# Kernel tuning notes

Measured on AMD Instinct MI355X. Metric: run time of the kernel, lower is better.

The kernel has to match this reference:

```python
import jax, jax.numpy as jnp
import numpy as np

S, B, D_IN, D_SRC, D_ALIGN = 2048, 64, 512, 512, 512


def setup_inputs() -> dict:
    key = jax.random.key(0)
    ks = jax.random.split(key, 6)
    scale = 0.1  # matches uniform_(-0.1, 0.1) init magnitude
    return {
        "input": jax.random.normal(ks[0], (1, B, D_IN), dtype=jnp.float32),
        "source_hids": jax.random.normal(ks[1], (S, B, D_SRC), dtype=jnp.float32),
        "encoder_padding_mask": jnp.zeros((S, B), dtype=bool),
        "W1": jax.random.uniform(ks[2], (D_ALIGN, D_IN + D_SRC), jnp.float32, -scale, scale),
        "b1": jax.random.uniform(ks[3], (D_ALIGN,), jnp.float32, -scale, scale),
        "W2": jax.random.uniform(ks[4], (1, D_ALIGN), jnp.float32, -scale, scale),
        "b2": jax.random.uniform(ks[5], (1,), jnp.float32, -scale, scale),
    }


def reference(input, source_hids, encoder_padding_mask, W1, b1, W2, b2):
    # input: [1, B, D_in] broadcast over srclen; source_hids: [S, B, D_src]
    s = source_hids.shape[0]
    x = jnp.broadcast_to(input, (s,) + input.shape[1:])          # [S, B, D_in]
    cat = jnp.concatenate((x, source_hids), axis=-1)             # [S, B, D_in+D_src]
    h = jnp.tanh(jnp.einsum('sbd,ad->sba', cat, W1) + b1)        # [S, B, D_align]
    scores = jnp.einsum('sba,oa->sbo', h, W2)[..., 0] + b2[0]    # [S, B]
    scores = jnp.where(encoder_padding_mask, -jnp.inf, scores)
    attn = jax.nn.softmax(scores, axis=0)                        # softmax over srclen
    ctx = jnp.einsum('sb,sbd->bd', attn, source_hids)            # [B, D_src]
    return ctx, attn
```

## Files before the change

### kernel.cpp

```cpp
#include <hip/hip_runtime.h>
#include <hip/hip_bf16.h>
#include <math.h>

#define S_LEN 2048
#define BATCH 64
#define DDIM 512

typedef __attribute__((ext_vector_type(8))) short bf16x8;
typedef __attribute__((ext_vector_type(4))) float f32x4;
typedef __attribute__((ext_vector_type(4))) unsigned int u32x4;

typedef __attribute__((address_space(1))) const void g_void;
typedef __attribute__((address_space(3))) void l_void;

__device__ __forceinline__ unsigned short f2bf(float f) {
  unsigned int u = __float_as_uint(f);
  u += 0x7fffu + ((u >> 16) & 1u);
  return (unsigned short)(u >> 16);
}

__device__ __forceinline__ float tanh_fast(float x) {
  float e = __builtin_amdgcn_exp2f(x * 2.88539008177793f);
  return 1.0f - 2.0f * __builtin_amdgcn_rcpf(e + 1.0f);
}

__device__ __forceinline__ unsigned pkbf(float a, float b) {
  unsigned ua = __float_as_uint(a) + 0x8000u;
  unsigned ub = __float_as_uint(b) + 0x8000u;
  return __builtin_amdgcn_perm(ub, ua, 0x07060302u);
}

__global__ __launch_bounds__(256) void prep_kernel(
    const float* __restrict__ W1, const float* __restrict__ b1,
    const float* __restrict__ input, unsigned short* __restrict__ W1b,
    float* __restrict__ uprime) {
  __shared__ float w1row[1024];
  const int a = blockIdx.x;
  const int t = threadIdx.x;
  float4 v = *(const float4*)(W1 + a * 1024 + t * 4);
  *(float4*)(w1row + t * 4) = v;
  if (t >= 128) {
    ushort4 u;
    u.x = f2bf(v.x); u.y = f2bf(v.y); u.z = f2bf(v.z); u.w = f2bf(v.w);
    *(ushort4*)(W1b + a * 512 + (t * 4 - 512)) = u;
  }
  __syncthreads();
  if (t < BATCH) {
    const float4* inp = (const float4*)(input + t * 512);
    const float4* wr = (const float4*)w1row;
    float acc = b1[a];
#pragma unroll 4
    for (int d = 0; d < 128; ++d) {
      float4 x = inp[d], w = wr[d];
      acc += x.x * w.x + x.y * w.y + x.z * w.z + x.w * w.w;
    }
    uprime[t * 512 + a] = acc;
  }
}

__global__ __launch_bounds__(512, 2) void scores_kernel(
    const float* __restrict__ src, const unsigned short* __restrict__ W1b,
    const float* __restrict__ uprime, const float* __restrict__ W2,
    float* __restrict__ scores_t) {
  __shared__ unsigned short A_sm[128 * 64];
  __shared__ unsigned short B_sm[2 * 512 * 64];
  __shared__ float s_lds[128];

  const int t = threadIdx.x;
  const int sblk = blockIdx.x;
  const int w = t >> 6;
  const int lane = t & 63;
  const int quad = lane >> 4;
  const int l15 = lane & 15;

  if (t < 128) s_lds[t] = 0.f;

  f32x4 acc[8][4];
#pragma unroll
  for (int i = 0; i < 8; ++i)
#pragma unroll
    for (int j = 0; j < 4; ++j) acc[i][j] = (f32x4){0.f, 0.f, 0.f, 0.f};

  const int ar = t >> 2, aq = t & 3;
  const float* gA = src + (size_t)(sblk * 128) * DDIM + ar * DDIM + aq * 16;
  const int p0 = (2 * aq) ^ (ar & 7);
  const int p1 = (2 * aq + 1) ^ (ar & 7);
  unsigned short* ldsA0 = A_sm + ar * 64 + p0 * 8;
  unsigned short* ldsA1 = A_sm + ar * 64 + p1 * 8;

  const int br = lane >> 3, bp = lane & 7, bc = bp ^ (br & 7);
  const unsigned short* gBl = W1b + br * DDIM + bc * 8;

  {
    float4 as0 = ((const float4*)gA)[0];
    float4 as1 = ((const float4*)gA)[1];
    float4 as2 = ((const float4*)gA)[2];
    float4 as3 = ((const float4*)gA)[3];
#pragma unroll
    for (int g = 0; g < 8; ++g) {
      const unsigned short* gp = gBl + (g * 64 + w * 8) * DDIM;
      unsigned short* lp = B_sm + (g * 64 + w * 8) * 64;
      __builtin_amdgcn_global_load_lds((g_void*)gp, (l_void*)lp, 16, 0, 0);
    }
    u32x4 o0, o1;
    o0.x = pkbf(as0.x, as0.y); o0.y = pkbf(as0.z, as0.w);
    o0.z = pkbf(as1.x, as1.y); o0.w = pkbf(as1.z, as1.w);
    o1.x = pkbf(as2.x, as2.y); o1.y = pkbf(as2.z, as2.w);
    o1.z = pkbf(as3.x, as3.y); o1.w = pkbf(as3.z, as3.w);
    *(u32x4*)ldsA0 = o0;
    *(u32x4*)ldsA1 = o1;
  }
  __syncthreads();

  for (int kt = 0; kt < 8; ++kt) {
    const int cur = kt & 1;
    const int pf = kt < 7;
    float4 as0, as1, as2, as3;
    if (pf) {
      const float4* gAn = (const float4*)(gA + (kt + 1) * 64);
      as0 = gAn[0]; as1 = gAn[1]; as2 = gAn[2]; as3 = gAn[3];
#pragma unroll
      for (int g = 0; g < 8; ++g) {
        const unsigned short* gp = gBl + (g * 64 + w * 8) * DDIM + (kt + 1) * 64;
        unsigned short* lp =
            B_sm + (cur ^ 1) * (512 * 64) + (g * 64 + w * 8) * 64;
        __builtin_amdgcn_global_load_lds((g_void*)gp, (l_void*)lp, 16, 0, 0);
      }
    }

    const unsigned short* Bc = B_sm + cur * (512 * 64);
#pragma unroll
    for (int ks = 0; ks < 2; ++ks) {
      const int c = ks * 4 + quad;
      bf16x8 af[8], bfr[4];
#pragma unroll
      for (int i = 0; i < 8; ++i) {
        const int r = i * 16 + l15;
        af[i] = *(const bf16x8*)(A_sm + r * 64 + ((c ^ (r & 7)) << 3));
      }
#pragma unroll
      for (int j = 0; j < 4; ++j) {
        const int n = w * 64 + j * 16 + l15;
        bfr[j] = *(const bf16x8*)(Bc + n * 64 + ((c ^ (n & 7)) << 3));
      }
#pragma unroll
      for (int i = 0; i < 8; ++i)
#pragma unroll
        for (int j = 0; j < 4; ++j)
          acc[i][j] = __builtin_amdgcn_mfma_f32_16x16x32_bf16(af[i], bfr[j],
                                                              acc[i][j], 0, 0, 0);
    }
    __syncthreads();

    if (pf) {
      u32x4 o0, o1;
      o0.x = pkbf(as0.x, as0.y); o0.y = pkbf(as0.z, as0.w);
      o0.z = pkbf(as1.x, as1.y); o0.w = pkbf(as1.z, as1.w);
      o1.x = pkbf(as2.x, as2.y); o1.y = pkbf(as2.z, as2.w);
      o1.z = pkbf(as3.x, as3.y); o1.w = pkbf(as3.z, as3.w);
      *(u32x4*)ldsA0 = o0;
      *(u32x4*)ldsA1 = o1;
    }
    __syncthreads();
  }

  float w2r[4];
#pragma unroll
  for (int j = 0; j < 4; ++j) w2r[j] = W2[w * 64 + j * 16 + l15];

#pragma unroll
  for (int i = 0; i < 8; ++i) {
#pragma unroll
    for (int r = 0; r < 4; ++r) {
      const int row = i * 16 + quad * 4 + r;
      const int b = row & 63;
      const int sl = row >> 6;
      const float* up = uprime + b * 512 + w * 64 + l15;
      float sp = 0.f;
#pragma unroll
      for (int j = 0; j < 4; ++j)
        sp += w2r[j] * tanh_fast(acc[i][j][r] + up[j * 16]);
      sp += __shfl_xor(sp, 1);
      sp += __shfl_xor(sp, 2);
      sp += __shfl_xor(sp, 4);
      sp += __shfl_xor(sp, 8);
      if (l15 == 0) atomicAdd(&s_lds[sl * 64 + b], sp);
    }
  }
  __syncthreads();
  if (t < 128)
    scores_t[(t & 63) * S_LEN + sblk * 2 + (t >> 6)] = s_lds[t];
}

__global__ __launch_bounds__(256) void softmax_kernel(
    const float* __restrict__ scores_t, const unsigned char* __restrict__ mask,
    float* __restrict__ attn_g, float* __restrict__ attn_t, int write_t) {
  __shared__ float red[256];
  const int b = blockIdx.x, t = threadIdx.x;
  float m = -__builtin_inff();
  float sc[8];
#pragma unroll
  for (int c = 0; c < 8; ++c) {
    const int s = t + c * 256;
    sc[c] = mask[s * BATCH + b] ? -__builtin_inff() : scores_t[b * S_LEN + s];
    m = fmaxf(m, sc[c]);
  }
  red[t] = m;
  __syncthreads();
  for (int off = 128; off; off >>= 1) {
    if (t < off) red[t] = fmaxf(red[t], red[t + off]);
    __syncthreads();
  }
  m = red[0];
  __syncthreads();
  float sum = 0.f;
#pragma unroll
  for (int c = 0; c < 8; ++c) sum += __expf(sc[c] - m);
  red[t] = sum;
  __syncthreads();
  for (int off = 128; off; off >>= 1) {
    if (t < off) red[t] += red[t + off];
    __syncthreads();
  }
  const float inv = 1.f / red[0];
#pragma unroll
  for (int c = 0; c < 8; ++c) {
    const int s = t + c * 256;
    const float p = __expf(sc[c] - m) * inv;
    attn_g[s * BATCH + b] = p;
    if (write_t) attn_t[b * S_LEN + s] = p;
  }
}

__global__ __launch_bounds__(256) void ctx_partial_kernel(
    const float* __restrict__ src, const float* __restrict__ attn_t,
    float* __restrict__ partial) {
  __shared__ float a_lds[64];
  const int c = blockIdx.x;
  const int b = blockIdx.y;
  const int t = threadIdx.x;
  if (t < 64) a_lds[t] = attn_t[b * S_LEN + c * 64 + t];
  __syncthreads();
  const int f4i = t & 127;
  const int sh = t >> 7;
  const float4* base =
      (const float4*)src + ((size_t)(c * 64 + sh * 32) * BATCH + b) * 128 + f4i;
  float4 acc = {0.f, 0.f, 0.f, 0.f};
#pragma unroll 8
  for (int i = 0; i < 32; ++i) {
    const float a = a_lds[sh * 32 + i];
    float4 v = base[(size_t)i * BATCH * 128];
    acc.x += a * v.x; acc.y += a * v.y; acc.z += a * v.z; acc.w += a * v.w;
  }
  ((float4*)partial)[((size_t)(c * 2 + sh) * BATCH + b) * 128 + f4i] = acc;
}

__global__ __launch_bounds__(256) void ctx_reduce_kernel(
    const float* __restrict__ partial, float* __restrict__ ctx) {
  const int b = blockIdx.x, t = threadIdx.x;
  const float2* p = (const float2*)partial + (size_t)b * 256 + t;
  float2 acc = {0.f, 0.f};
#pragma unroll 8
  for (int c2 = 0; c2 < 64; ++c2) {
    float2 v = p[(size_t)c2 * BATCH * 256];
    acc.x += v.x; acc.y += v.y;
  }
  ((float2*)ctx)[b * 256 + t] = acc;
}

__global__ __launch_bounds__(256) void ctx_atomic_kernel(
    const float* __restrict__ src, const float* __restrict__ attn_g,
    float* __restrict__ ctx) {
  __shared__ float a_lds[128];
  const int s0 = blockIdx.x * 128, b = blockIdx.y, t = threadIdx.x;
  if (t < 128) a_lds[t] = attn_g[(s0 + t) * BATCH + b];
  __syncthreads();
  const int f4i = t & 127;
  const int sh = t >> 7;
  const float4* base =
      (const float4*)src + ((size_t)(s0 + sh * 64) * BATCH + b) * 128 + f4i;
  float4 acc = {0.f, 0.f, 0.f, 0.f};
#pragma unroll 8
  for (int i = 0; i < 64; ++i) {
    const float a = a_lds[sh * 64 + i];
    float4 v = base[(size_t)i * BATCH * 128];
    acc.x += a * v.x; acc.y += a * v.y; acc.z += a * v.z; acc.w += a * v.w;
  }
  float* cp = ctx + b * DDIM + f4i * 4;
  atomicAdd(cp + 0, acc.x);
  atomicAdd(cp + 1, acc.y);
  atomicAdd(cp + 2, acc.z);
  atomicAdd(cp + 3, acc.w);
}

extern "C" void kernel_launch(void* const* d_in, const int* in_sizes, int n_in,
                              void* d_out, int out_size, void* d_ws, size_t ws_size,
                              hipStream_t stream) {
  const float* input = (const float*)d_in[0];
  const float* src = (const float*)d_in[1];
  const unsigned char* mask = (const unsigned char*)d_in[2];
  const float* W1 = (const float*)d_in[3];
  const float* b1 = (const float*)d_in[4];
  const float* W2 = (const float*)d_in[5];

  float* ctx = (float*)d_out;
  float* attn = (float*)d_out + BATCH * DDIM;

  unsigned short* W1b = (unsigned short*)d_ws;
  float* uprime = (float*)((char*)d_ws + 512 * 1024);
  float* scores_t = (float*)((char*)d_ws + 640 * 1024);
  float* attn_t = (float*)((char*)d_ws + 1152 * 1024);
  float* partial = (float*)((char*)d_ws + 1664 * 1024);
  const size_t NEED_ATTN_T = 1664 * 1024;
  const size_t NEED_PARTIAL = 1664 * 1024 + (size_t)64 * BATCH * DDIM * 4;
  const int have_attn_t = ws_size >= NEED_ATTN_T;
  const int have_partial = ws_size >= NEED_PARTIAL;

  prep_kernel<<<512, 256, 0, stream>>>(W1, b1, input, W1b, uprime);
  scores_kernel<<<S_LEN / 2, 512, 0, stream>>>(src, W1b, uprime, W2, scores_t);
  softmax_kernel<<<BATCH, 256, 0, stream>>>(scores_t, mask, attn, attn_t,
                                            have_attn_t && have_partial);
  if (have_partial) {
    ctx_partial_kernel<<<dim3(32, BATCH), 256, 0, stream>>>(src, attn_t, partial);
    ctx_reduce_kernel<<<BATCH, 256, 0, stream>>>(partial, ctx);
  } else {
    hipMemsetAsync(ctx, 0, BATCH * DDIM * sizeof(float), stream);
    ctx_atomic_kernel<<<dim3(16, BATCH), 256, 0, stream>>>(src, attn, ctx);
  }
}
```

Measured before the change: 505.7 us.

## Load W1 fragments directly from global in MFMA layout, double-buffer A tile

The prep kernel now writes bf16 W1 in a k-chunk-major layout, so each lane can read its MFMA B fragment with one contiguous 16-byte global load. This removes the LDS staging of the 512x64 W1 tile. The freed LDS is used to double-buffer the source (A) tile, which drops one barrier per k-step. In exchange, every block re-reads W1 from global or L2 instead of sharing it through LDS, and those load latencies are exposed right before the MFMAs.

```diff
diff --git a/kernel.cpp b/kernel.cpp
--- a/kernel.cpp
+++ b/kernel.cpp
@@ -9,9 +9,6 @@
 typedef __attribute__((ext_vector_type(8))) short bf16x8;
 typedef __attribute__((ext_vector_type(4))) float f32x4;
 typedef __attribute__((ext_vector_type(4))) unsigned int u32x4;
-
-typedef __attribute__((address_space(1))) const void g_void;
-typedef __attribute__((address_space(3))) void l_void;
 
 __device__ __forceinline__ unsigned short f2bf(float f) {
   unsigned int u = __float_as_uint(f);
@@ -32,7 +29,7 @@
 
 __global__ __launch_bounds__(256) void prep_kernel(
     const float* __restrict__ W1, const float* __restrict__ b1,
-    const float* __restrict__ input, unsigned short* __restrict__ W1b,
+    const float* __restrict__ input, unsigned short* __restrict__ W1bT,
     float* __restrict__ uprime) {
   __shared__ float w1row[1024];
   const int a = blockIdx.x;
@@ -42,7 +39,10 @@
   if (t >= 128) {
     ushort4 u;
     u.x = f2bf(v.x); u.y = f2bf(v.y); u.z = f2bf(v.z); u.w = f2bf(v.w);
-    *(ushort4*)(W1b + a * 512 + (t * 4 - 512)) = u;
+    const int d = t * 4 - 512;
+    const int kc = d >> 3;
+    const int e = d & 7;
+    *(ushort4*)(W1bT + ((size_t)kc * 512 + a) * 8 + e) = u;
   }
   __syncthreads();
   if (t < BATCH) {
@@ -59,11 +59,10 @@
 }
 
 __global__ __launch_bounds__(512, 2) void scores_kernel(
-    const float* __restrict__ src, const unsigned short* __restrict__ W1b,
+    const float* __restrict__ src, const unsigned short* __restrict__ W1bT,
     const float* __restrict__ uprime, const float* __restrict__ W2,
     float* __restrict__ scores_t) {
-  __shared__ unsigned short A_sm[128 * 64];
-  __shared__ unsigned short B_sm[2 * 512 * 64];
+  __shared__ unsigned short A_sm[2][128 * 64];
   __shared__ float s_lds[128];
 
   const int t = threadIdx.x;
@@ -85,72 +84,62 @@
   const float* gA = src + (size_t)(sblk * 128) * DDIM + ar * DDIM + aq * 16;
   const int p0 = (2 * aq) ^ (ar & 7);
   const int p1 = (2 * aq + 1) ^ (ar & 7);
-  unsigned short* ldsA0 = A_sm + ar * 64 + p0 * 8;
-  unsigned short* ldsA1 = A_sm + ar * 64 + p1 * 8;
-
-  const int br = lane >> 3, bp = lane & 7, bc = bp ^ (br & 7);
-  const unsigned short* gBl = W1b + br * DDIM + bc * 8;
+  const int ldsA0 = ar * 64 + p0 * 8;
+  const int ldsA1 = ar * 64 + p1 * 8;
+
+  const int ncol = w * 64 + l15;
 
   {
     float4 as0 = ((const float4*)gA)[0];
     float4 as1 = ((const float4*)gA)[1];
     float4 as2 = ((const float4*)gA)[2];
     float4 as3 = ((const float4*)gA)[3];
-#pragma unroll
-    for (int g = 0; g < 8; ++g) {
-      const unsigned short* gp = gBl + (g * 64 + w * 8) * DDIM;
-      unsigned short* lp = B_sm + (g * 64 + w * 8) * 64;
-      __builtin_amdgcn_global_load_lds((g_void*)gp, (l_void*)lp, 16, 0, 0);
-    }
     u32x4 o0, o1;
     o0.x = pkbf(as0.x, as0.y); o0.y = pkbf(as0.z, as0.w);
     o0.z = pkbf(as1.x, as1.y); o0.w = pkbf(as1.z, as1.w);
     o1.x = pkbf(as2.x, as2.y); o1.y = pkbf(as2.z, as2.w);
     o1.z = pkbf(as3.x, as3.y); o1.w = pkbf(as3.z, as3.w);
-    *(u32x4*)ldsA0 = o0;
-    *(u32x4*)ldsA1 = o1;
+    *(u32x4*)(A_sm[0] + ldsA0) = o0;
+    *(u32x4*)(A_sm[0] + ldsA1) = o1;
   }
   __syncthreads();
 
   for (int kt = 0; kt < 8; ++kt) {
     const int cur = kt & 1;
-    const int pf = kt < 7;
+    const bool pf = kt < 7;
     float4 as0, as1, as2, as3;
     if (pf) {
       const float4* gAn = (const float4*)(gA + (kt + 1) * 64);
       as0 = gAn[0]; as1 = gAn[1]; as2 = gAn[2]; as3 = gAn[3];
-#pragma unroll
-      for (int g = 0; g < 8; ++g) {
-        const unsigned short* gp = gBl + (g * 64 + w * 8) * DDIM + (kt + 1) * 64;
-        unsigned short* lp =
-            B_sm + (cur ^ 1) * (512 * 64) + (g * 64 + w * 8) * 64;
-        __builtin_amdgcn_global_load_lds((g_void*)gp, (l_void*)lp, 16, 0, 0);
+    }
+
+    bf16x8 bb[2][4];
+#pragma unroll
+    for (int ks = 0; ks < 2; ++ks)
+#pragma unroll
+      for (int j = 0; j < 4; ++j) {
+        const int kc = kt * 8 + ks * 4 + quad;
+        bb[ks][j] =
+            *(const bf16x8*)(W1bT + ((size_t)kc * 512 + ncol + j * 16) * 8);
       }
-    }
-
-    const unsigned short* Bc = B_sm + cur * (512 * 64);
+
+    const unsigned short* Ac = A_sm[cur];
 #pragma unroll
     for (int ks = 0; ks < 2; ++ks) {
       const int c = ks * 4 + quad;
-      bf16x8 af[8], bfr[4];
+      bf16x8 af[8];
 #pragma unroll
       for (int i = 0; i < 8; ++i) {
         const int r = i * 16 + l15;
-        af[i] = *(const bf16x8*)(A_sm + r * 64 + ((c ^ (r & 7)) << 3));
+        af[i] = *(const bf16x8*)(Ac + r * 64 + ((c ^ (r & 7)) << 3));
       }
 #pragma unroll
-      for (int j = 0; j < 4; ++j) {
-        const int n = w * 64 + j * 16 + l15;
-        bfr[j] = *(const bf16x8*)(Bc + n * 64 + ((c ^ (n & 7)) << 3));
-      }
-#pragma unroll
       for (int i = 0; i < 8; ++i)
 #pragma unroll
         for (int j = 0; j < 4; ++j)
-          acc[i][j] = __builtin_amdgcn_mfma_f32_16x16x32_bf16(af[i], bfr[j],
+          acc[i][j] = __builtin_amdgcn_mfma_f32_16x16x32_bf16(af[i], bb[ks][j],
                                                               acc[i][j], 0, 0, 0);
     }
-    __syncthreads();
 
     if (pf) {
       u32x4 o0, o1;
@@ -158,8 +147,8 @@
       o0.z = pkbf(as1.x, as1.y); o0.w = pkbf(as1.z, as1.w);
       o1.x = pkbf(as2.x, as2.y); o1.y = pkbf(as2.z, as2.w);
       o1.z = pkbf(as3.x, as3.y); o1.w = pkbf(as3.z, as3.w);
-      *(u32x4*)ldsA0 = o0;
-      *(u32x4*)ldsA1 = o1;
+      *(u32x4*)(A_sm[cur ^ 1] + ldsA0) = o0;
+      *(u32x4*)(A_sm[cur ^ 1] + ldsA1) = o1;
     }
     __syncthreads();
   }
@@ -306,7 +295,7 @@
   float* ctx = (float*)d_out;
   float* attn = (float*)d_out + BATCH * DDIM;
 
-  unsigned short* W1b = (unsigned short*)d_ws;
+  unsigned short* W1bT = (unsigned short*)d_ws;
   float* uprime = (float*)((char*)d_ws + 512 * 1024);
   float* scores_t = (float*)((char*)d_ws + 640 * 1024);
   float* attn_t = (float*)((char*)d_ws + 1152 * 1024);
@@ -316,8 +305,8 @@
   const int have_attn_t = ws_size >= NEED_ATTN_T;
   const int have_partial = ws_size >= NEED_PARTIAL;
 
-  prep_kernel<<<512, 256, 0, stream>>>(W1, b1, input, W1b, uprime);
-  scores_kernel<<<S_LEN / 2, 512, 0, stream>>>(src, W1b, uprime, W2, scores_t);
+  prep_kernel<<<512, 256, 0, stream>>>(W1, b1, input, W1bT, uprime);
+  scores_kernel<<<S_LEN / 2, 512, 0, stream>>>(src, W1bT, uprime, W2, scores_t);
   softmax_kernel<<<BATCH, 256, 0, stream>>>(scores_t, mask, attn, attn_t,
                                             have_attn_t && have_partial);
   if (have_partial) {
```

Result: no change. 502.7 us (-0.6%).
